# Performance work log

Hardware: AMD Instinct MI355X
Metric: run time of the kernel (lower is better)

Reference implementation:

```python
import jax, jax.numpy as jnp
import numpy as np
import itertools

KS = 5           # kernel_size per pseudo dim
PDIM = 2         # pseudo-coordinate dim
N_NODES = 50000
N_EDGES = 800000
D_IN = 128
D_OUT = 128
EPS = 1e-12


def l2norm(x):
    n = jnp.linalg.norm(x, axis=-1, keepdims=True)
    return x / jnp.maximum(n, EPS)


def spline_conv(x, src, dst, pseudo, weight, bias):
    """torch_spline_conv with degree=1, open splines, aggr='mean', no root weight."""
    N = x.shape[0]
    out_dim = weight.shape[-1]
    dim = pseudo.shape[1]
    v = pseudo * (KS - 1)                                   # [E, dim] in [0, KS-1)
    i0 = jnp.clip(jnp.floor(v), 0, KS - 2).astype(jnp.int32)
    frac = v - i0.astype(v.dtype)                           # [E, dim]
    # Precompute per-kernel transforms once per node: cheaper than per-edge GEMV
    Xk = jnp.einsum('ni,kio->nko', x, weight)               # [N, K=25, out]
    E = src.shape[0]
    y = jnp.zeros((E, out_dim), x.dtype)
    for bits in itertools.product((0, 1), repeat=dim):      # S = 2**dim = 4 combos
        b = jnp.ones((E,), x.dtype)
        wi = jnp.zeros((E,), jnp.int32)
        stride = 1
        for d, bit in enumerate(bits):
            b = b * (frac[:, d] if bit else 1.0 - frac[:, d])
            wi = wi + (i0[:, d] + bit) * stride
            stride *= KS
        y = y + b[:, None] * Xk[src, wi]                    # gather-weight per edge
    agg = jax.ops.segment_sum(y, dst, num_segments=N)       # scatter-add to targets
    deg = jax.ops.segment_sum(jnp.ones((E,), x.dtype), dst, num_segments=N)
    return agg / jnp.maximum(deg, 1.0)[:, None] + bias      # mean aggregation


def setup_inputs() -> dict:
    key = jax.random.key(0)
    ks = jax.random.split(key, 6)
    K = KS ** PDIM
    x = jax.random.normal(ks[0], (N_NODES, D_IN), jnp.float32)
    edge_index = jax.random.randint(ks[1], (2, N_EDGES), 0, N_NODES, jnp.int32)
    edge_attr = jax.random.uniform(ks[2], (N_EDGES, PDIM), jnp.float32)
    s0 = 1.0 / np.sqrt(K * D_IN)
    s1 = 1.0 / np.sqrt(K * D_OUT)
    w0 = jax.random.normal(ks[3], (K, D_IN, D_OUT), jnp.float32) * s0
    w1 = jax.random.normal(ks[4], (K, D_OUT, D_OUT), jnp.float32) * s1
    b0 = jnp.zeros((D_OUT,), jnp.float32)
    b1 = jnp.zeros((D_OUT,), jnp.float32)
    return {"x": x, "edge_index": edge_index, "edge_attr": edge_attr,
            "w0": w0, "b0": b0, "w1": w1, "b1": b1}


def reference(x, edge_index, edge_attr, w0, b0, w1, b1):
    src, dst = edge_index[0], edge_index[1]
    xs = [l2norm(x)]
    h = x
    for w, b in ((w0, b0), (w1, b1)):
        h = spline_conv(h, src, dst, edge_attr, w, b)
        xs.append(l2norm(h))
        h = jax.nn.relu(h)
    return jnp.concatenate(xs, axis=-1)                     # [N, D_IN + 2*D_OUT]
```

## Files before the change

kernel.cpp:

```cpp
#include <hip/hip_runtime.h>

#define D     128
#define OD    384
#define NK    25
#define KCMAX 13

typedef __attribute__((ext_vector_type(8))) short bf16x8;
typedef __attribute__((ext_vector_type(4))) float f32x4;
typedef const __attribute__((address_space(1))) void gv_t;
typedef __attribute__((address_space(3))) void lv_t;

struct __align__(16) Rec {
  int src;
  unsigned int wi;
  unsigned int b01;
  unsigned int b23;
};

__device__ inline unsigned short f2bf(float f) {
  unsigned int u = __float_as_uint(f);
  u += 0x7fffu + ((u >> 16) & 1u);
  return (unsigned short)(u >> 16);
}
__device__ inline unsigned short f2h(float f) {
  return __builtin_bit_cast(unsigned short, (_Float16)f);
}
__device__ inline float h2f(unsigned int bits16) {
  return (float)__builtin_bit_cast(_Float16, (unsigned short)(bits16 & 0xffffu));
}


__global__ __launch_bounds__(256) void deg_kernel(const int* __restrict__ dstA, int E,
                                                  int* __restrict__ deg) {
  int e = blockIdx.x * 256 + threadIdx.x;
  if (e < E) atomicAdd(&deg[dstA[e]], 1);
}

__global__ __launch_bounds__(1024) void scan_kernel(const int* __restrict__ deg, int N,
                                                    int* __restrict__ base) {
  __shared__ int part[1024];
  int tid = threadIdx.x;
  int chunk = (N + 1023) / 1024;
  int s0 = min(N, tid * chunk), s1 = min(N, s0 + chunk);
  int sum = 0;
  for (int i = s0; i < s1; ++i) sum += deg[i];
  part[tid] = sum;
  __syncthreads();
  if (tid == 0) {
    int acc = 0;
    for (int i = 0; i < 1024; ++i) { int t = part[i]; part[i] = acc; acc += t; }
  }
  __syncthreads();
  int acc = part[tid];
  for (int i = s0; i < s1; ++i) { base[i] = acc; acc += deg[i]; }
}

__global__ __launch_bounds__(256) void fill_kernel(const int* __restrict__ srcA,
    const int* __restrict__ dstA, const float* __restrict__ attr, int E,
    const int* __restrict__ base, int* __restrict__ cursor, Rec* __restrict__ recs) {
  int e = blockIdx.x * 256 + threadIdx.x;
  if (e >= E) return;
  int d = dstA[e];
  int pos = base[d] + atomicAdd(&cursor[d], 1);
  float v0 = attr[2 * e] * 4.0f;
  float v1 = attr[2 * e + 1] * 4.0f;
  int i0 = min(3, max(0, (int)v0));
  int i1 = min(3, max(0, (int)v1));
  float f0 = v0 - (float)i0;
  float f1 = v1 - (float)i1;
  Rec r;
  r.src = srcA[e];
  unsigned int w00 = (unsigned int)(i0 + 5 * i1);
  r.wi = w00 | ((w00 + 1) << 5) | ((w00 + 5) << 10) | ((w00 + 6) << 15);
  r.b01 = (unsigned int)f2h((1.f - f0) * (1.f - f1)) | ((unsigned int)f2h(f0 * (1.f - f1)) << 16);
  r.b23 = (unsigned int)f2h((1.f - f0) * f1) | ((unsigned int)f2h(f0 * f1) << 16);
  recs[pos] = r;
}

__global__ __launch_bounds__(256) void wt_kernel(const float* __restrict__ W,
                                                 unsigned short* __restrict__ WT) {
  int idx = blockIdx.x * 256 + threadIdx.x;
  if (idx >= 128 * NK * D) return;
  int n = idx / (NK * D);
  int kk = idx - n * (NK * D);
  WT[idx] = f2bf(W[(size_t)kk * D + n]);
}


__global__ __launch_bounds__(256) void gather_kernel(const int* __restrict__ base,
    const int* __restrict__ deg, const Rec* __restrict__ recs,
    const unsigned short* __restrict__ Xb, unsigned short* __restrict__ Gc, int N,
    int KCc, int kc0) {
  __shared__ float lacc[4][KCMAX * D];
  int w = threadIdx.x >> 6, l = threadIdx.x & 63;
  int dst = blockIdx.x * 4 + w;
  if (dst >= N) return;
  float* A = lacc[w];
  for (int k = 0; k < KCc; ++k)
    *(float2*)(A + k * D + l * 2) = make_float2(0.f, 0.f);

  auto ACC = [&](const Rec& r, unsigned int xp) {
    float x0 = __uint_as_float(xp << 16);
    float x1 = __uint_as_float(xp & 0xffff0000u);
    float bq[4] = {h2f(r.b01), h2f(r.b01 >> 16), h2f(r.b23), h2f(r.b23 >> 16)};
#pragma unroll
    for (int q = 0; q < 4; ++q) {
      int k = (int)((r.wi >> (5 * q)) & 31u) - kc0;
      if ((unsigned)k < (unsigned)KCc) {
        float2 p = *(const float2*)(A + k * D + l * 2);
        p.x = fmaf(bq[q], x0, p.x);
        p.y = fmaf(bq[q], x1, p.y);
        *(float2*)(A + k * D + l * 2) = p;
      }
    }
  };

  int s = base[dst], e = s + deg[dst];
  int j = s;
  for (; j + 3 < e; j += 4) {
    Rec r0 = recs[j], r1 = recs[j + 1], r2 = recs[j + 2], r3 = recs[j + 3];
    unsigned int xp0 = *(const unsigned int*)(Xb + (size_t)r0.src * D + l * 2);
    unsigned int xp1 = *(const unsigned int*)(Xb + (size_t)r1.src * D + l * 2);
    unsigned int xp2 = *(const unsigned int*)(Xb + (size_t)r2.src * D + l * 2);
    unsigned int xp3 = *(const unsigned int*)(Xb + (size_t)r3.src * D + l * 2);
    ACC(r0, xp0); ACC(r1, xp1); ACC(r2, xp2); ACC(r3, xp3);
  }
  for (; j < e; ++j) {
    Rec r = recs[j];
    unsigned int xp = *(const unsigned int*)(Xb + (size_t)r.src * D + l * 2);
    ACC(r, xp);
  }

  unsigned short* gr = Gc + (size_t)dst * ((size_t)KCc * D);
  for (int k = 0; k < KCc; ++k) {
    float2 v = *(const float2*)(A + k * D + l * 2);
    unsigned int pk = (unsigned int)f2bf(v.x) | ((unsigned int)f2bf(v.y) << 16);
    *(unsigned int*)(gr + k * D + l * 2) = pk;
  }
}


__global__ __launch_bounds__(256) void gemm_kernel(
    const unsigned short* __restrict__ G, const unsigned short* __restrict__ WT,
    float* __restrict__ Y, int N, int KCc, int kc0, int first) {
  __shared__ __attribute__((aligned(16))) char At[2][16384];
  __shared__ __attribute__((aligned(16))) char Bt[2][16384];
  const int tid = threadIdx.x;
  const int w = tid >> 6;
  const int l = tid & 63;
  const int m0 = blockIdx.x * 128;
  const size_t ldG = (size_t)KCc * 256;
  const size_t ldW = (size_t)NK * 256;

  const int lrow = l >> 3;
  const int scol = ((l & 7) * 16) ^ (lrow << 4);

  f32x4 acc[2][8];
#pragma unroll
  for (int mr = 0; mr < 2; ++mr)
#pragma unroll
    for (int nc = 0; nc < 8; ++nc) {
      if (first) {
        acc[mr][nc] = (f32x4){0.f, 0.f, 0.f, 0.f};
      } else {
        int col = nc * 16 + (l & 15);
#pragma unroll
        for (int j = 0; j < 4; ++j) {
          int row = m0 + w * 32 + mr * 16 + (l >> 4) * 4 + j;
          acc[mr][nc][j] = (row < N) ? Y[(size_t)row * D + col] : 0.f;
        }
      }
    }

  const int steps = KCc * 2;
  auto STAGE = [&](int kt, int b) {
#pragma unroll
    for (int i = 0; i < 4; ++i) {
      int row = w * 32 + i * 8 + lrow;
      int node = m0 + row;
      if (node > N - 1) node = N - 1;
      const char* src = (const char*)G + (size_t)node * ldG + kt * 128 + scol;
      __builtin_amdgcn_global_load_lds((gv_t*)src, (lv_t*)(At[b] + (w * 4 + i) * 1024),
                                       16, 0, 0);
    }
#pragma unroll
    for (int i = 0; i < 4; ++i) {
      int nr = w * 32 + i * 8 + lrow;
      const char* src = (const char*)WT + (size_t)nr * ldW + kc0 * 256 + kt * 128 + scol;
      __builtin_amdgcn_global_load_lds((gv_t*)src, (lv_t*)(Bt[b] + (w * 4 + i) * 1024),
                                       16, 0, 0);
    }
  };

  STAGE(0, 0);
  __syncthreads();
  for (int kt = 0; kt < steps; ++kt) {
    const int cur = kt & 1;
    if (kt + 1 < steps) STAGE(kt + 1, cur ^ 1);
#pragma unroll
    for (int ks = 0; ks < 2; ++ks) {
      int kb = ks * 64 + (l >> 4) * 16;
      bf16x8 a[2], b[8];
#pragma unroll
      for (int mr = 0; mr < 2; ++mr) {
        int r = w * 32 + mr * 16 + (l & 15);
        a[mr] = *(const bf16x8*)(At[cur] + r * 128 + (kb ^ ((r & 7) << 4)));
      }
#pragma unroll
      for (int nc = 0; nc < 8; ++nc) {
        int nr = nc * 16 + (l & 15);
        b[nc] = *(const bf16x8*)(Bt[cur] + nr * 128 + (kb ^ ((nr & 7) << 4)));
      }
#pragma unroll
      for (int mr = 0; mr < 2; ++mr)
#pragma unroll
        for (int nc = 0; nc < 8; ++nc)
          acc[mr][nc] =
              __builtin_amdgcn_mfma_f32_16x16x32_bf16(a[mr], b[nc], acc[mr][nc], 0, 0, 0);
    }
    __syncthreads();
  }

#pragma unroll
  for (int mr = 0; mr < 2; ++mr)
#pragma unroll
    for (int nc = 0; nc < 8; ++nc) {
      int col = nc * 16 + (l & 15);
#pragma unroll
      for (int j = 0; j < 4; ++j) {
        int row = m0 + w * 32 + mr * 16 + (l >> 4) * 4 + j;
        if (row < N) Y[(size_t)row * D + col] = acc[mr][nc][j];
      }
    }
}


__global__ __launch_bounds__(256) void l2norm_x_kernel(const float* __restrict__ x,
    float* __restrict__ out, unsigned short* __restrict__ xbf, int N) {
  int g = blockIdx.x * 256 + threadIdx.x;
  int n = g >> 6, lane = g & 63;
  if (n >= N) return;
  float2 v = *(const float2*)(x + (size_t)n * D + lane * 2);
  float ss = v.x * v.x + v.y * v.y;
#pragma unroll
  for (int m = 1; m < 64; m <<= 1) ss += __shfl_xor(ss, m, 64);
  float r = 1.0f / fmaxf(sqrtf(ss), 1e-12f);
  *(float2*)(out + (size_t)n * OD + lane * 2) = make_float2(v.x * r, v.y * r);
  unsigned int pk = (unsigned int)f2bf(v.x) | ((unsigned int)f2bf(v.y) << 16);
  *(unsigned int*)(xbf + (size_t)n * D + lane * 2) = pk;
}

__global__ __launch_bounds__(256) void finalize_kernel(const float* __restrict__ y,
    const int* __restrict__ deg, const float* __restrict__ bias, float* __restrict__ out,
    unsigned short* __restrict__ xnext, int N) {
  int g = blockIdx.x * 256 + threadIdx.x;
  int n = g >> 6, lane = g & 63;
  if (n >= N) return;
  float inv = 1.0f / (float)max(deg[n], 1);
  float2 a = *(const float2*)(y + (size_t)n * D + lane * 2);
  float2 b = *(const float2*)(bias + lane * 2);
  float h0 = a.x * inv + b.x;
  float h1 = a.y * inv + b.y;
  float ss = h0 * h0 + h1 * h1;
#pragma unroll
  for (int m = 1; m < 64; m <<= 1) ss += __shfl_xor(ss, m, 64);
  float r = 1.0f / fmaxf(sqrtf(ss), 1e-12f);
  *(float2*)(out + (size_t)n * OD + lane * 2) = make_float2(h0 * r, h1 * r);
  if (xnext) {
    unsigned int pk = (unsigned int)f2bf(fmaxf(h0, 0.f)) |
                      ((unsigned int)f2bf(fmaxf(h1, 0.f)) << 16);
    *(unsigned int*)(xnext + (size_t)n * D + lane * 2) = pk;
  }
}


extern "C" void kernel_launch(void* const* d_in, const int* in_sizes, int n_in,
                              void* d_out, int out_size, void* d_ws, size_t ws_size,
                              hipStream_t stream) {
  const float* x    = (const float*)d_in[0];
  const int*   ei   = (const int*)d_in[1];
  const float* attr = (const float*)d_in[2];
  const float* w0   = (const float*)d_in[3];
  const float* b0   = (const float*)d_in[4];
  const float* w1   = (const float*)d_in[5];
  const float* b1   = (const float*)d_in[6];
  float* out = (float*)d_out;

  const int N = in_sizes[0] / D;
  const int E = in_sizes[1] / 2;
  const int* srcA = ei;
  const int* dstA = ei + E;

  char* p = (char*)d_ws;
  auto carve = [&](size_t bytes) -> char* {
    char* r = p;
    p += (bytes + 255) & ~(size_t)255;
    return r;
  };
  unsigned short* xbf    = (unsigned short*)carve((size_t)N * D * 2);
  unsigned short* xtmp   = (unsigned short*)carve((size_t)N * D * 2);
  float*          ygemm  = (float*)carve((size_t)N * D * 4);
  int*            deg    = (int*)carve((size_t)N * 4);
  int*            base   = (int*)carve((size_t)N * 4);
  int*            cursor = (int*)carve((size_t)N * 4);
  Rec*            recs   = (Rec*)carve((size_t)E * sizeof(Rec));
  unsigned short* WT0    = (unsigned short*)carve((size_t)128 * NK * D * 2);
  unsigned short* WT1    = (unsigned short*)carve((size_t)128 * NK * D * 2);
  size_t used = (size_t)(p - (char*)d_ws);
  size_t remain = (ws_size > used) ? (ws_size - used) : 0;
  int KCg = (int)(remain / ((size_t)N * D * 2));
  if (KCg > KCMAX) KCg = KCMAX;
  if (KCg < 1) KCg = 1;
  unsigned short* Gc = (unsigned short*)carve((size_t)N * (size_t)KCg * D * 2);
  (void)n_in; (void)out_size;

  hipMemsetAsync(deg, 0, (size_t)N * 4, stream);
  hipMemsetAsync(cursor, 0, (size_t)N * 4, stream);

  int eb = (E + 255) / 256;
  deg_kernel<<<eb, 256, 0, stream>>>(dstA, E, deg);
  scan_kernel<<<1, 1024, 0, stream>>>(deg, N, base);
  fill_kernel<<<eb, 256, 0, stream>>>(srcA, dstA, attr, E, base, cursor, recs);
  int wtb = (128 * NK * D + 255) / 256;
  wt_kernel<<<wtb, 256, 0, stream>>>(w0, WT0);
  wt_kernel<<<wtb, 256, 0, stream>>>(w1, WT1);

  int nb = (N * 64 + 255) / 256;
  l2norm_x_kernel<<<nb, 256, 0, stream>>>(x, out, xbf, N);

  int gbg = (N + 3) / 4;
  int gbm = (N + 127) / 128;
  const unsigned short* xin = xbf;
  const float* Bv[2] = {b0, b1};
  const unsigned short* WTl[2] = {WT0, WT1};
  for (int layer = 0; layer < 2; ++layer) {
    int first = 1;
    for (int kc0 = 0; kc0 < NK; kc0 += KCg) {
      int KCc = min(KCg, NK - kc0);
      gather_kernel<<<gbg, 256, 0, stream>>>(base, deg, recs, xin, Gc, N, KCc, kc0);
      gemm_kernel<<<gbm, 256, 0, stream>>>(Gc, WTl[layer], ygemm, N, KCc, kc0, first);
      first = 0;
    }
    finalize_kernel<<<nb, 256, 0, stream>>>(ygemm, deg, Bv[layer], out + D * (layer + 1),
                                            layer == 0 ? xtmp : nullptr, N);
    xin = xtmp;
  }
}
```

Before: 762.3 us.

## Sort edges per destination by kernel-chunk class to skip irrelevant edges in gather

Edges of each destination are bucketed into three classes by which half of the 25 spline kernels their four weight indices touch, using a per-(node,class) count, scan and fill. Each of the two gather passes then visits only the edge ranges that can contribute to its chunk, instead of scanning every edge twice. The write-back of accumulators is also widened to 16-byte stores. In exchange, the edge-sorting kernels count and scan three times as many entries (a 150K-entry single-block scan), and the chunk split is now fixed at 13 kernels when the workspace allows it.

```diff
diff --git a/kernel.cpp b/kernel.cpp
--- a/kernel.cpp
+++ b/kernel.cpp
@@ -4,9 +4,11 @@
 #define OD    384
 #define NK    25
 #define KCMAX 13
+#define KB0   13
 
 typedef __attribute__((ext_vector_type(8))) short bf16x8;
 typedef __attribute__((ext_vector_type(4))) float f32x4;
+typedef __attribute__((ext_vector_type(4))) unsigned int u32x4;
 typedef const __attribute__((address_space(1))) void gv_t;
 typedef __attribute__((address_space(3))) void lv_t;
 
@@ -30,20 +32,33 @@
 }
 
 
-__global__ __launch_bounds__(256) void deg_kernel(const int* __restrict__ dstA, int E,
-                                                  int* __restrict__ deg) {
+__device__ inline int edge_cls(int w00) {
+  return (w00 + 6 < KB0) ? 0 : ((w00 >= KB0) ? 2 : 1);
+}
+
+__global__ __launch_bounds__(256) void count3_kernel(const int* __restrict__ dstA,
+    const float* __restrict__ attr, int E, int* __restrict__ deg,
+    int* __restrict__ cnt3) {
   int e = blockIdx.x * 256 + threadIdx.x;
-  if (e < E) atomicAdd(&deg[dstA[e]], 1);
-}
-
-__global__ __launch_bounds__(1024) void scan_kernel(const int* __restrict__ deg, int N,
-                                                    int* __restrict__ base) {
+  if (e >= E) return;
+  int d = dstA[e];
+  atomicAdd(&deg[d], 1);
+  float v0 = attr[2 * e] * 4.0f;
+  float v1 = attr[2 * e + 1] * 4.0f;
+  int i0 = min(3, max(0, (int)v0));
+  int i1 = min(3, max(0, (int)v1));
+  int w00 = i0 + 5 * i1;
+  atomicAdd(&cnt3[d * 3 + edge_cls(w00)], 1);
+}
+
+__global__ __launch_bounds__(1024) void scan_kernel(const int* __restrict__ cnt, int M,
+    int* __restrict__ base3, int* __restrict__ cursor) {
   __shared__ int part[1024];
   int tid = threadIdx.x;
-  int chunk = (N + 1023) / 1024;
-  int s0 = min(N, tid * chunk), s1 = min(N, s0 + chunk);
+  int chunk = (M + 1023) / 1024;
+  int s0 = min(M, tid * chunk), s1 = min(M, s0 + chunk);
   int sum = 0;
-  for (int i = s0; i < s1; ++i) sum += deg[i];
+  for (int i = s0; i < s1; ++i) sum += cnt[i];
   part[tid] = sum;
   __syncthreads();
   if (tid == 0) {
@@ -52,26 +67,28 @@
   }
   __syncthreads();
   int acc = part[tid];
-  for (int i = s0; i < s1; ++i) { base[i] = acc; acc += deg[i]; }
+  for (int i = s0; i < s1; ++i) { base3[i] = acc; cursor[i] = acc; acc += cnt[i]; }
+  if (tid == 1023) base3[M] = acc;
 }
 
 __global__ __launch_bounds__(256) void fill_kernel(const int* __restrict__ srcA,
     const int* __restrict__ dstA, const float* __restrict__ attr, int E,
-    const int* __restrict__ base, int* __restrict__ cursor, Rec* __restrict__ recs) {
+    int* __restrict__ cursor, Rec* __restrict__ recs) {
   int e = blockIdx.x * 256 + threadIdx.x;
   if (e >= E) return;
   int d = dstA[e];
-  int pos = base[d] + atomicAdd(&cursor[d], 1);
   float v0 = attr[2 * e] * 4.0f;
   float v1 = attr[2 * e + 1] * 4.0f;
   int i0 = min(3, max(0, (int)v0));
   int i1 = min(3, max(0, (int)v1));
   float f0 = v0 - (float)i0;
   float f1 = v1 - (float)i1;
+  int w00 = i0 + 5 * i1;
+  int pos = atomicAdd(&cursor[d * 3 + edge_cls(w00)], 1);
   Rec r;
   r.src = srcA[e];
-  unsigned int w00 = (unsigned int)(i0 + 5 * i1);
-  r.wi = w00 | ((w00 + 1) << 5) | ((w00 + 5) << 10) | ((w00 + 6) << 15);
+  unsigned int w = (unsigned int)w00;
+  r.wi = w | ((w + 1) << 5) | ((w + 5) << 10) | ((w + 6) << 15);
   r.b01 = (unsigned int)f2h((1.f - f0) * (1.f - f1)) | ((unsigned int)f2h(f0 * (1.f - f1)) << 16);
   r.b23 = (unsigned int)f2h((1.f - f0) * f1) | ((unsigned int)f2h(f0 * f1) << 16);
   recs[pos] = r;
@@ -87,10 +104,9 @@
 }
 
 
-__global__ __launch_bounds__(256) void gather_kernel(const int* __restrict__ base,
-    const int* __restrict__ deg, const Rec* __restrict__ recs,
-    const unsigned short* __restrict__ Xb, unsigned short* __restrict__ Gc, int N,
-    int KCc, int kc0) {
+__global__ __launch_bounds__(256) void gather_kernel(const int* __restrict__ base3,
+    const Rec* __restrict__ recs, const unsigned short* __restrict__ Xb,
+    unsigned short* __restrict__ Gc, int N, int KCc, int kc0, int c_lo, int c_hi) {
   __shared__ float lacc[4][KCMAX * D];
   int w = threadIdx.x >> 6, l = threadIdx.x & 63;
   int dst = blockIdx.x * 4 + w;
@@ -115,7 +131,8 @@
     }
   };
 
-  int s = base[dst], e = s + deg[dst];
+  int s = __builtin_amdgcn_readfirstlane(base3[dst * 3 + c_lo]);
+  int e = __builtin_amdgcn_readfirstlane(base3[dst * 3 + c_hi]);
   int j = s;
   for (; j + 3 < e; j += 4) {
     Rec r0 = recs[j], r1 = recs[j + 1], r2 = recs[j + 2], r3 = recs[j + 3];
@@ -132,10 +149,16 @@
   }
 
   unsigned short* gr = Gc + (size_t)dst * ((size_t)KCc * D);
-  for (int k = 0; k < KCc; ++k) {
-    float2 v = *(const float2*)(A + k * D + l * 2);
-    unsigned int pk = (unsigned int)f2bf(v.x) | ((unsigned int)f2bf(v.y) << 16);
-    *(unsigned int*)(gr + k * D + l * 2) = pk;
+  for (int t = l; t < KCc * 16; t += 64) {
+    const float* src = A + (t >> 4) * D + (t & 15) * 8;
+    float4 v0 = *(const float4*)(src);
+    float4 v1 = *(const float4*)(src + 4);
+    u32x4 pk;
+    pk[0] = (unsigned int)f2bf(v0.x) | ((unsigned int)f2bf(v0.y) << 16);
+    pk[1] = (unsigned int)f2bf(v0.z) | ((unsigned int)f2bf(v0.w) << 16);
+    pk[2] = (unsigned int)f2bf(v1.x) | ((unsigned int)f2bf(v1.y) << 16);
+    pk[3] = (unsigned int)f2bf(v1.z) | ((unsigned int)f2bf(v1.w) << 16);
+    *(u32x4*)(gr + (size_t)t * 8) = pk;
   }
 }
 
@@ -301,8 +324,9 @@
   unsigned short* xtmp   = (unsigned short*)carve((size_t)N * D * 2);
   float*          ygemm  = (float*)carve((size_t)N * D * 4);
   int*            deg    = (int*)carve((size_t)N * 4);
-  int*            base   = (int*)carve((size_t)N * 4);
-  int*            cursor = (int*)carve((size_t)N * 4);
+  int*            cnt3   = (int*)carve((size_t)N * 3 * 4);
+  int*            base3  = (int*)carve(((size_t)N * 3 + 1) * 4);
+  int*            cursor = (int*)carve((size_t)N * 3 * 4);
   Rec*            recs   = (Rec*)carve((size_t)E * sizeof(Rec));
   unsigned short* WT0    = (unsigned short*)carve((size_t)128 * NK * D * 2);
   unsigned short* WT1    = (unsigned short*)carve((size_t)128 * NK * D * 2);
@@ -315,12 +339,12 @@
   (void)n_in; (void)out_size;
 
   hipMemsetAsync(deg, 0, (size_t)N * 4, stream);
-  hipMemsetAsync(cursor, 0, (size_t)N * 4, stream);
+  hipMemsetAsync(cnt3, 0, (size_t)N * 3 * 4, stream);
 
   int eb = (E + 255) / 256;
-  deg_kernel<<<eb, 256, 0, stream>>>(dstA, E, deg);
-  scan_kernel<<<1, 1024, 0, stream>>>(deg, N, base);
-  fill_kernel<<<eb, 256, 0, stream>>>(srcA, dstA, attr, E, base, cursor, recs);
+  count3_kernel<<<eb, 256, 0, stream>>>(dstA, attr, E, deg, cnt3);
+  scan_kernel<<<1, 1024, 0, stream>>>(cnt3, N * 3, base3, cursor);
+  fill_kernel<<<eb, 256, 0, stream>>>(srcA, dstA, attr, E, cursor, recs);
   int wtb = (128 * NK * D + 255) / 256;
   wt_kernel<<<wtb, 256, 0, stream>>>(w0, WT0);
   wt_kernel<<<wtb, 256, 0, stream>>>(w1, WT1);
@@ -334,12 +358,19 @@
   const float* Bv[2] = {b0, b1};
   const unsigned short* WTl[2] = {WT0, WT1};
   for (int layer = 0; layer < 2; ++layer) {
-    int first = 1;
-    for (int kc0 = 0; kc0 < NK; kc0 += KCg) {
-      int KCc = min(KCg, NK - kc0);
-      gather_kernel<<<gbg, 256, 0, stream>>>(base, deg, recs, xin, Gc, N, KCc, kc0);
-      gemm_kernel<<<gbm, 256, 0, stream>>>(Gc, WTl[layer], ygemm, N, KCc, kc0, first);
-      first = 0;
+    if (KCg >= KB0) {
+      gather_kernel<<<gbg, 256, 0, stream>>>(base3, recs, xin, Gc, N, KB0, 0, 0, 2);
+      gemm_kernel<<<gbm, 256, 0, stream>>>(Gc, WTl[layer], ygemm, N, KB0, 0, 1);
+      gather_kernel<<<gbg, 256, 0, stream>>>(base3, recs, xin, Gc, N, NK - KB0, KB0, 1, 3);
+      gemm_kernel<<<gbm, 256, 0, stream>>>(Gc, WTl[layer], ygemm, N, NK - KB0, KB0, 0);
+    } else {
+      int first = 1;
+      for (int kc0 = 0; kc0 < NK; kc0 += KCg) {
+        int KCc = min(KCg, NK - kc0);
+        gather_kernel<<<gbg, 256, 0, stream>>>(base3, recs, xin, Gc, N, KCc, kc0, 0, 3);
+        gemm_kernel<<<gbm, 256, 0, stream>>>(Gc, WTl[layer], ygemm, N, KCc, kc0, first);
+        first = 0;
+      }
     }
     finalize_kernel<<<nb, 256, 0, stream>>>(ygemm, deg, Bv[layer], out + D * (layer + 1),
                                             layer == 0 ? xtmp : nullptr, N);
```

Result: slower. 955.1 us (+25.3%).
